# Optimization experiments

Hardware: AMD Instinct MI355X
Metric: run time of the kernel (lower is better)

The kernel has to match this reference:

```python
import jax, jax.numpy as jnp
import numpy as np

B, H, S, D = 2, 16, 2048, 64

def setup_inputs() -> dict:
    key = jax.random.key(0)
    kq, kk, kv = jax.random.split(key, 3)
    q = jax.random.normal(kq, (B, H, S, D), dtype=jnp.float32)
    k = jax.random.normal(kk, (B, H, S, D), dtype=jnp.float32)
    v = jax.random.normal(kv, (B, H, S, D), dtype=jnp.float32)
    # additive causal mask: 0 on/below diagonal, -1e9 above
    causal = jnp.tril(jnp.ones((S, S), dtype=bool))
    mask = jnp.where(causal, 0.0, -1e9).astype(jnp.float32)[None, None]
    return {"q": q, "k": k, "v": v, "mask": mask}

def reference(q, k, v, mask):
    # scores: [B,H,Sq,Sk]
    scale = 1.0 / jnp.sqrt(jnp.asarray(k.shape[-1], dtype=q.dtype))
    scores = jnp.einsum("bhqd,bhkd->bhqk", q, k) * scale
    scores = scores + mask
    attn = jax.nn.softmax(scores, axis=-1)
    return jnp.einsum("bhqk,bhkd->bhqd", attn, v)
```

## Files before the change

kernel.cpp:

```cpp
#include <hip/hip_runtime.h>
#include <hip/hip_bf16.h>


#define S_LEN 2048
#define D_DIM 64
#define BQ 64
#define BKV 64
#define NQT (S_LEN / BQ)
#define NBH 32

typedef __bf16 bf16x8 __attribute__((ext_vector_type(8)));
typedef __bf16 bf16x4 __attribute__((ext_vector_type(4)));
typedef float f32x4 __attribute__((ext_vector_type(4)));

#define QSCALE 0.1803368801111243f
#define NEG_INF (-1e30f)
#define THRLOG2 11.5f

__device__ inline void glds16(const void* g, void* l) {
    __builtin_amdgcn_global_load_lds(
        (const __attribute__((address_space(1))) unsigned int*)g,
        (__attribute__((address_space(3))) unsigned int*)l, 16, 0, 0);
}

__device__ inline float m3(float a, float b, float c) {
    return fmaxf(fmaxf(a, b), c);
}

__global__ __launch_bounds__(256)
void conv_fused_kernel(const float* __restrict__ k, const float* __restrict__ v,
                       __bf16* __restrict__ kb, __bf16* __restrict__ vt)
{
    __shared__ __bf16 T[64][72];
    const int bh = blockIdx.y, st = blockIdx.x;
    const int tid = threadIdx.x;
    const size_t base = (size_t)bh * S_LEN * D_DIM + (size_t)st * 64 * D_DIM;
    const float* kh = k + base;
    const float* vh = v + base;
    __bf16* kbh = kb + base;

#pragma unroll
    for (int it = 0; it < 2; ++it) {
        size_t i = ((size_t)tid + it * 256) * 8;
        float4 a = *(const float4*)(kh + i);
        float4 b = *(const float4*)(kh + i + 4);
        bf16x8 o;
        o[0] = (__bf16)a.x; o[1] = (__bf16)a.y; o[2] = (__bf16)a.z; o[3] = (__bf16)a.w;
        o[4] = (__bf16)b.x; o[5] = (__bf16)b.y; o[6] = (__bf16)b.z; o[7] = (__bf16)b.w;
        *(bf16x8*)(kbh + i) = o;
    }

#pragma unroll
    for (int it = 0; it < 4; ++it) {
        int idx = tid + it * 256;
        int s = idx >> 4, c4 = idx & 15;
        float4 f = *(const float4*)(vh + s * D_DIM + c4 * 4);
        T[c4 * 4 + 0][s] = (__bf16)f.x;
        T[c4 * 4 + 1][s] = (__bf16)f.y;
        T[c4 * 4 + 2][s] = (__bf16)f.z;
        T[c4 * 4 + 3][s] = (__bf16)f.w;
    }
    __syncthreads();
    __bf16* vth = vt + (size_t)bh * D_DIM * S_LEN + st * 64;
#pragma unroll
    for (int it = 0; it < 2; ++it) {
        int idx = tid + it * 256;
        int d = idx >> 3, c8 = idx & 7;
        int kk = c8 >> 2, g = c8 & 3;
        bf16x4 v0 = *(const bf16x4*)&T[d][kk * 32 + 4 * g];
        bf16x4 v1 = *(const bf16x4*)&T[d][kk * 32 + 16 + 4 * g];
        bf16x8 o;
        o[0] = v0[0]; o[1] = v0[1]; o[2] = v0[2]; o[3] = v0[3];
        o[4] = v1[0]; o[5] = v1[1]; o[6] = v1[2]; o[7] = v1[3];
        *(bf16x8*)(vth + (size_t)d * S_LEN + c8 * 8) = o;
    }
}


__global__ __launch_bounds__(256)
void attn_fwd_glds(const float* __restrict__ q, const __bf16* __restrict__ kb,
                   const __bf16* __restrict__ vt, float* __restrict__ out)
{
    __shared__ __bf16 KL[3][64][64];
    __shared__ __bf16 VL[3][64][64];

    const int tid  = threadIdx.x;
    const int w    = tid >> 6;
    const int lane = tid & 63;
    const int l15  = lane & 15;
    const int lg   = lane >> 4;

    const int p  = blockIdx.x;
    const int bh = blockIdx.y;

    const float*  qh = q  + (size_t)bh * S_LEN * D_DIM;
    const __bf16* kh = kb + (size_t)bh * S_LEN * D_DIM;
    const __bf16* vh = vt + (size_t)bh * D_DIM * S_LEN;
    float*        oh = out + (size_t)bh * S_LEN * D_DIM;

    int row_u[2], scol_u[2];
#pragma unroll
    for (int u = 0; u < 2; ++u) {
        int e = (u * 4 + w) * 512 + lane * 8;
        int r = e >> 6, c0 = e & 63;
        row_u[u]  = r;
        scol_u[u] = c0 ^ ((r & 7) << 3);
    }

#define STAGE(kt, buf)                                                          \
    {                                                                           \
        _Pragma("unroll")                                                       \
        for (int u = 0; u < 2; ++u) {                                           \
            glds16(kh + (size_t)((kt) * BKV + row_u[u]) * D_DIM + scol_u[u],    \
                   (__bf16*)&KL[buf][0][0] + (u * 4 + w) * 512);                \
            glds16(vh + (size_t)row_u[u] * S_LEN + (kt) * BKV + scol_u[u],      \
                   (__bf16*)&VL[buf][0][0] + (u * 4 + w) * 512);                \
        }                                                                       \
    }

    for (int half = 0; half < 2; ++half) {
        const int qtile = (half == 0) ? (NQT - 1 - p) : p;
        const int qbase = qtile * BQ;
        const int nt    = qtile + 1;

        bf16x8 qf[2];
        {
            const int qrow = qbase + w * 16 + l15;
            const float* qp = qh + (size_t)qrow * D_DIM + 8 * lg;
#pragma unroll
            for (int kk = 0; kk < 2; ++kk) {
                float4 a = *(const float4*)(qp + kk * 32);
                float4 b = *(const float4*)(qp + kk * 32 + 4);
                bf16x8 f;
                f[0] = (__bf16)(a.x * QSCALE); f[1] = (__bf16)(a.y * QSCALE);
                f[2] = (__bf16)(a.z * QSCALE); f[3] = (__bf16)(a.w * QSCALE);
                f[4] = (__bf16)(b.x * QSCALE); f[5] = (__bf16)(b.y * QSCALE);
                f[6] = (__bf16)(b.z * QSCALE); f[7] = (__bf16)(b.w * QSCALE);
                qf[kk] = f;
            }
        }

        f32x4 acc[4] = {};
        float m_run = NEG_INF;
        float l_part = 0.0f;

        if (half == 1) __syncthreads();
        STAGE(0, 0);
        if (nt > 1) STAGE(1, 1);

        for (int kt = 0; kt < nt; ++kt) {
            const int cur = kt % 3;
            if (kt + 1 < nt) { asm volatile("s_waitcnt vmcnt(4)" ::: "memory"); }
            else             { asm volatile("s_waitcnt vmcnt(0)" ::: "memory"); }
            __builtin_amdgcn_s_barrier();
            if (kt + 2 < nt) STAGE(kt + 2, (kt + 2) % 3);

            f32x4 s[4];
            __builtin_amdgcn_s_setprio(1);
#pragma unroll
            for (int jt = 0; jt < 4; ++jt) {
                const int j  = jt * 16 + l15;
                const int sw = (j & 7) << 3;
                f32x4 c = {};
#pragma unroll
                for (int kk = 0; kk < 2; ++kk) {
                    bf16x8 kf = *(const bf16x8*)&KL[cur][j][(kk * 32 + 8 * lg) ^ sw];
                    c = __builtin_amdgcn_mfma_f32_16x16x32_bf16(kf, qf[kk], c, 0, 0, 0);
                }
                s[jt] = c;
            }
            __builtin_amdgcn_s_setprio(0);

            if (kt == qtile) {
                const int qin = w * 16 + l15;
#pragma unroll
                for (int jt = 0; jt < 4; ++jt)
#pragma unroll
                    for (int r = 0; r < 4; ++r)
                        if (jt * 16 + 4 * lg + r > qin) s[jt][r] = NEG_INF;
            }

            float t0 = m3(s[0][0], s[0][1], s[0][2]);
            float t1 = m3(s[0][3], s[1][0], s[1][1]);
            float t2 = m3(s[1][2], s[1][3], s[2][0]);
            float t3 = m3(s[2][1], s[2][2], s[2][3]);
            float t4 = m3(s[3][0], s[3][1], s[3][2]);
            float mxl = m3(m3(t0, t1, t2), m3(t3, t4, s[3][3]), NEG_INF);

            if (__any(mxl > m_run + THRLOG2)) {
                float mx = fmaxf(mxl, __shfl_xor(mxl, 16));
                mx = fmaxf(mx, __shfl_xor(mx, 32));
                const float mt   = fmaxf(m_run, mx);
                const float corr = __builtin_amdgcn_exp2f(m_run - mt);
                l_part *= corr;
                m_run   = mt;
                float corr_a[4];
#pragma unroll
                for (int r = 0; r < 4; ++r) corr_a[r] = __shfl(corr, 4 * lg + r);
#pragma unroll
                for (int dt = 0; dt < 4; ++dt)
#pragma unroll
                    for (int r = 0; r < 4; ++r) acc[dt][r] *= corr_a[r];
            }

            float ps = 0.0f;
            float pe[4][4];
#pragma unroll
            for (int jt = 0; jt < 4; ++jt)
#pragma unroll
                for (int r = 0; r < 4; ++r) {
                    float e = __builtin_amdgcn_exp2f(s[jt][r] - m_run);
                    pe[jt][r] = e;
                    ps += e;
                }
            l_part += ps;

            bf16x8 pa[2];
#pragma unroll
            for (int kk = 0; kk < 2; ++kk)
#pragma unroll
                for (int i = 0; i < 4; ++i) {
                    pa[kk][i]     = (__bf16)pe[2 * kk][i];
                    pa[kk][4 + i] = (__bf16)pe[2 * kk + 1][i];
                }

            __builtin_amdgcn_s_setprio(1);
#pragma unroll
            for (int dt = 0; dt < 4; ++dt) {
                const int d  = dt * 16 + l15;
                const int sw = (d & 7) << 3;
#pragma unroll
                for (int kk = 0; kk < 2; ++kk) {
                    bf16x8 vb = *(const bf16x8*)&VL[cur][d][(kk * 32 + 8 * lg) ^ sw];
                    acc[dt] = __builtin_amdgcn_mfma_f32_16x16x32_bf16(pa[kk], vb, acc[dt], 0, 0, 0);
                }
            }
            __builtin_amdgcn_s_setprio(0);
        }

        float l_tot = l_part + __shfl_xor(l_part, 16);
        l_tot += __shfl_xor(l_tot, 32);
        float li_a[4];
#pragma unroll
        for (int r = 0; r < 4; ++r)
            li_a[r] = __builtin_amdgcn_rcpf(__shfl(l_tot, 4 * lg + r));
#pragma unroll
        for (int dt = 0; dt < 4; ++dt)
#pragma unroll
            for (int r = 0; r < 4; ++r)
                oh[(size_t)(qbase + w * 16 + 4 * lg + r) * D_DIM + dt * 16 + l15] =
                    acc[dt][r] * li_a[r];
    }
#undef STAGE
}


#define PAD 72
__global__ __launch_bounds__(256)
void attn_fwd_fallback(const float* __restrict__ q, const float* __restrict__ k,
                       const float* __restrict__ v, float* __restrict__ out)
{
    __shared__ __bf16 Klds[BKV][PAD];
    __shared__ __bf16 Vt[D_DIM][PAD];
    __shared__ __bf16 Plds[4][16][PAD];

    const int tid  = threadIdx.x;
    const int w    = tid >> 6;
    const int lane = tid & 63;
    const int l15  = lane & 15;
    const int lg   = lane >> 4;

    const int qtile = blockIdx.x;
    const int bh    = blockIdx.y;
    const int qbase = qtile * BQ;

    const size_t head_off = (size_t)bh * S_LEN * D_DIM;
    const float* qh = q + head_off;
    const float* kh = k + head_off;
    const float* vh = v + head_off;
    float*       oh = out + head_off;

    bf16x8 qf[2];
    {
        const int qrow = qbase + w * 16 + l15;
        const float* qp = qh + (size_t)qrow * D_DIM + 8 * lg;
#pragma unroll
        for (int c = 0; c < 2; ++c) {
            float4 a = *(const float4*)(qp + c * 32);
            float4 b = *(const float4*)(qp + c * 32 + 4);
            bf16x8 f;
            f[0] = (__bf16)(a.x * 0.125f); f[1] = (__bf16)(a.y * 0.125f);
            f[2] = (__bf16)(a.z * 0.125f); f[3] = (__bf16)(a.w * 0.125f);
            f[4] = (__bf16)(b.x * 0.125f); f[5] = (__bf16)(b.y * 0.125f);
            f[6] = (__bf16)(b.z * 0.125f); f[7] = (__bf16)(b.w * 0.125f);
            qf[c] = f;
        }
    }

    f32x4 acc[4] = {};
    float m_run[4], l_run[4];
#pragma unroll
    for (int r = 0; r < 4; ++r) { m_run[r] = -1e30f; l_run[r] = 0.0f; }

    const int nkv = qtile + 1;
    for (int kt = 0; kt < nkv; ++kt) {
        const int kv0 = kt * BKV;
        __syncthreads();
#pragma unroll
        for (int it = 0; it < 4; ++it) {
            int idx = tid + it * 256;
            int row = idx >> 4;
            int c4  = idx & 15;
            float4 kf = *(const float4*)(kh + (size_t)(kv0 + row) * D_DIM + c4 * 4);
            __bf16* kd = &Klds[row][c4 * 4];
            kd[0] = (__bf16)kf.x; kd[1] = (__bf16)kf.y;
            kd[2] = (__bf16)kf.z; kd[3] = (__bf16)kf.w;
            float4 vf = *(const float4*)(vh + (size_t)(kv0 + row) * D_DIM + c4 * 4);
            Vt[c4 * 4 + 0][row] = (__bf16)vf.x;
            Vt[c4 * 4 + 1][row] = (__bf16)vf.y;
            Vt[c4 * 4 + 2][row] = (__bf16)vf.z;
            Vt[c4 * 4 + 3][row] = (__bf16)vf.w;
        }
        __syncthreads();

        f32x4 sfrag[4];
#pragma unroll
        for (int kc = 0; kc < 4; ++kc) {
            bf16x8 kf0 = *(const bf16x8*)&Klds[kc * 16 + l15][8 * lg];
            bf16x8 kf1 = *(const bf16x8*)&Klds[kc * 16 + l15][32 + 8 * lg];
            f32x4 c = {};
            c = __builtin_amdgcn_mfma_f32_16x16x32_bf16(qf[0], kf0, c, 0, 0, 0);
            c = __builtin_amdgcn_mfma_f32_16x16x32_bf16(qf[1], kf1, c, 0, 0, 0);
            sfrag[kc] = c;
        }

        if (kt == qtile) {
#pragma unroll
            for (int kc = 0; kc < 4; ++kc) {
                const int j = kv0 + kc * 16 + l15;
#pragma unroll
                for (int r = 0; r < 4; ++r) {
                    const int qrow = qbase + w * 16 + lg * 4 + r;
                    if (j > qrow) sfrag[kc][r] = -1e30f;
                }
            }
        }

        float mt[4], corr[4], ps[4];
#pragma unroll
        for (int r = 0; r < 4; ++r) {
            float mx = fmaxf(fmaxf(sfrag[0][r], sfrag[1][r]),
                             fmaxf(sfrag[2][r], sfrag[3][r]));
            mx = fmaxf(mx, __shfl_xor(mx, 1));
            mx = fmaxf(mx, __shfl_xor(mx, 2));
            mx = fmaxf(mx, __shfl_xor(mx, 4));
            mx = fmaxf(mx, __shfl_xor(mx, 8));
            mt[r]   = fmaxf(m_run[r], mx);
            corr[r] = __expf(m_run[r] - mt[r]);
            ps[r]   = 0.0f;
        }
#pragma unroll
        for (int kc = 0; kc < 4; ++kc) {
#pragma unroll
            for (int r = 0; r < 4; ++r) {
                float pp = __expf(sfrag[kc][r] - mt[r]);
                ps[r] += pp;
                Plds[w][lg * 4 + r][kc * 16 + l15] = (__bf16)pp;
            }
        }
#pragma unroll
        for (int r = 0; r < 4; ++r) {
            ps[r] += __shfl_xor(ps[r], 1);
            ps[r] += __shfl_xor(ps[r], 2);
            ps[r] += __shfl_xor(ps[r], 4);
            ps[r] += __shfl_xor(ps[r], 8);
            l_run[r] = l_run[r] * corr[r] + ps[r];
            m_run[r] = mt[r];
        }
#pragma unroll
        for (int dt = 0; dt < 4; ++dt)
#pragma unroll
            for (int r = 0; r < 4; ++r)
                acc[dt][r] *= corr[r];

#pragma unroll
        for (int kk = 0; kk < 2; ++kk) {
            bf16x8 pf = *(const bf16x8*)&Plds[w][l15][kk * 32 + 8 * lg];
#pragma unroll
            for (int dt = 0; dt < 4; ++dt) {
                bf16x8 vf = *(const bf16x8*)&Vt[dt * 16 + l15][kk * 32 + 8 * lg];
                acc[dt] = __builtin_amdgcn_mfma_f32_16x16x32_bf16(pf, vf, acc[dt], 0, 0, 0);
            }
        }
    }

#pragma unroll
    for (int dt = 0; dt < 4; ++dt) {
#pragma unroll
        for (int r = 0; r < 4; ++r) {
            const int qrow = qbase + w * 16 + lg * 4 + r;
            oh[(size_t)qrow * D_DIM + dt * 16 + l15] = acc[dt][r] / l_run[r];
        }
    }
}

extern "C" void kernel_launch(void* const* d_in, const int* in_sizes, int n_in,
                              void* d_out, int out_size, void* d_ws, size_t ws_size,
                              hipStream_t stream) {
    const float* q = (const float*)d_in[0];
    const float* k = (const float*)d_in[1];
    const float* v = (const float*)d_in[2];
    float* out = (float*)d_out;

    const size_t kv_elems  = (size_t)NBH * S_LEN * D_DIM;
    const size_t ws_needed = kv_elems * 2 * sizeof(__bf16);

    if (ws_size >= ws_needed) {
        __bf16* kb = (__bf16*)d_ws;
        __bf16* vt = kb + kv_elems;
        conv_fused_kernel<<<dim3(S_LEN / 64, NBH), dim3(256), 0, stream>>>(k, v, kb, vt);
        attn_fwd_glds<<<dim3(NQT / 2, NBH), dim3(256), 0, stream>>>(q, kb, vt, out);
    } else {
        attn_fwd_fallback<<<dim3(NQT, NBH), dim3(256), 0, stream>>>(q, k, v, out);
    }
}
```

Baseline: 57.12 us.

## Split KV loop across two blocks per query tile and add combine kernel

Adds a split-KV path in which each query-tile pair is handled by two blocks, each taking alternating KV tiles (even or odd). Each block writes unnormalized partial outputs plus row max and sum to workspace. A new combine kernel then merges the two partials using log-sum-exp rescaling. This doubles the grid to 1024 blocks so more CUs are busy, at the cost of an extra launch, extra global traffic for the partials, and a shallower double-buffered prefetch with a full vmcnt(0) wait each iteration.

```diff
diff --git a/kernel.cpp b/kernel.cpp
--- a/kernel.cpp
+++ b/kernel.cpp
@@ -77,36 +77,6 @@
 }
 
 
-__global__ __launch_bounds__(256)
-void attn_fwd_glds(const float* __restrict__ q, const __bf16* __restrict__ kb,
-                   const __bf16* __restrict__ vt, float* __restrict__ out)
-{
-    __shared__ __bf16 KL[3][64][64];
-    __shared__ __bf16 VL[3][64][64];
-
-    const int tid  = threadIdx.x;
-    const int w    = tid >> 6;
-    const int lane = tid & 63;
-    const int l15  = lane & 15;
-    const int lg   = lane >> 4;
-
-    const int p  = blockIdx.x;
-    const int bh = blockIdx.y;
-
-    const float*  qh = q  + (size_t)bh * S_LEN * D_DIM;
-    const __bf16* kh = kb + (size_t)bh * S_LEN * D_DIM;
-    const __bf16* vh = vt + (size_t)bh * D_DIM * S_LEN;
-    float*        oh = out + (size_t)bh * S_LEN * D_DIM;
-
-    int row_u[2], scol_u[2];
-#pragma unroll
-    for (int u = 0; u < 2; ++u) {
-        int e = (u * 4 + w) * 512 + lane * 8;
-        int r = e >> 6, c0 = e & 63;
-        row_u[u]  = r;
-        scol_u[u] = c0 ^ ((r & 7) << 3);
-    }
-
 #define STAGE(kt, buf)                                                          \
     {                                                                           \
         _Pragma("unroll")                                                       \
@@ -118,10 +88,42 @@
         }                                                                       \
     }
 
+__global__ __launch_bounds__(256)
+void attn_fwd_split(const float* __restrict__ q, const __bf16* __restrict__ kb,
+                    const __bf16* __restrict__ vt, float* __restrict__ opart,
+                    float* __restrict__ ml)
+{
+    __shared__ __bf16 KL[2][64][64];
+    __shared__ __bf16 VL[2][64][64];
+
+    const int tid  = threadIdx.x;
+    const int w    = tid >> 6;
+    const int lane = tid & 63;
+    const int l15  = lane & 15;
+    const int lg   = lane >> 4;
+
+    const int ph = blockIdx.x;
+    const int p  = ph >> 1;
+    const int h  = ph & 1;
+    const int bh = blockIdx.y;
+
+    const float*  qh = q  + (size_t)bh * S_LEN * D_DIM;
+    const __bf16* kh = kb + (size_t)bh * S_LEN * D_DIM;
+    const __bf16* vh = vt + (size_t)bh * D_DIM * S_LEN;
+
+    int row_u[2], scol_u[2];
+#pragma unroll
+    for (int u = 0; u < 2; ++u) {
+        int e = (u * 4 + w) * 512 + lane * 8;
+        int r = e >> 6, c0 = e & 63;
+        row_u[u]  = r;
+        scol_u[u] = c0 ^ ((r & 7) << 3);
+    }
+
     for (int half = 0; half < 2; ++half) {
         const int qtile = (half == 0) ? (NQT - 1 - p) : p;
         const int qbase = qtile * BQ;
-        const int nt    = qtile + 1;
+        const int cnt   = (qtile >= h) ? (((qtile - h) >> 1) + 1) : 0;
 
         bf16x8 qf[2];
         {
@@ -145,15 +147,14 @@
         float l_part = 0.0f;
 
         if (half == 1) __syncthreads();
-        STAGE(0, 0);
-        if (nt > 1) STAGE(1, 1);
-
-        for (int kt = 0; kt < nt; ++kt) {
-            const int cur = kt % 3;
-            if (kt + 1 < nt) { asm volatile("s_waitcnt vmcnt(4)" ::: "memory"); }
-            else             { asm volatile("s_waitcnt vmcnt(0)" ::: "memory"); }
+        if (cnt > 0) STAGE(h, 0);
+
+        for (int i = 0; i < cnt; ++i) {
+            const int kt  = h + 2 * i;
+            const int cur = i & 1;
+            asm volatile("s_waitcnt vmcnt(0)" ::: "memory");
             __builtin_amdgcn_s_barrier();
-            if (kt + 2 < nt) STAGE(kt + 2, (kt + 2) % 3);
+            if (i + 1 < cnt) STAGE(kt + 2, cur ^ 1);
 
             f32x4 s[4];
             __builtin_amdgcn_s_setprio(1);
@@ -219,6 +220,211 @@
 #pragma unroll
             for (int kk = 0; kk < 2; ++kk)
 #pragma unroll
+                for (int i2 = 0; i2 < 4; ++i2) {
+                    pa[kk][i2]     = (__bf16)pe[2 * kk][i2];
+                    pa[kk][4 + i2] = (__bf16)pe[2 * kk + 1][i2];
+                }
+
+            __builtin_amdgcn_s_setprio(1);
+#pragma unroll
+            for (int dt = 0; dt < 4; ++dt) {
+                const int d  = dt * 16 + l15;
+                const int sw = (d & 7) << 3;
+#pragma unroll
+                for (int kk = 0; kk < 2; ++kk) {
+                    bf16x8 vb = *(const bf16x8*)&VL[cur][d][(kk * 32 + 8 * lg) ^ sw];
+                    acc[dt] = __builtin_amdgcn_mfma_f32_16x16x32_bf16(pa[kk], vb, acc[dt], 0, 0, 0);
+                }
+            }
+            __builtin_amdgcn_s_setprio(0);
+        }
+
+        float l_tot = l_part + __shfl_xor(l_part, 16);
+        l_tot += __shfl_xor(l_tot, 32);
+
+        float* op = opart + ((((size_t)bh * NQT + qtile) * 2 + h) << 12);
+#pragma unroll
+        for (int dt = 0; dt < 4; ++dt)
+#pragma unroll
+            for (int r = 0; r < 4; ++r)
+                op[(w * 16 + 4 * lg + r) * 64 + dt * 16 + l15] = acc[dt][r];
+
+        if (lg == 0) {
+            float* mlp = ml + ((((size_t)bh * NQT + qtile) * 2 + h) << 7);
+            mlp[w * 16 + l15]      = m_run;
+            mlp[64 + w * 16 + l15] = l_tot;
+        }
+    }
+}
+
+
+__global__ __launch_bounds__(256)
+void combine_kernel(const float* __restrict__ opart, const float* __restrict__ ml,
+                    float* __restrict__ out)
+{
+    const int qt  = blockIdx.x;
+    const int bh  = blockIdx.y;
+    const int tid = threadIdx.x;
+    const int row = tid >> 2;
+    const int c16 = (tid & 3) * 16;
+
+    const float* ml0 = ml + ((((size_t)bh * NQT + qt) * 2) << 7);
+    const float* ml1 = ml0 + 128;
+    const float m0 = ml0[row], l0 = ml0[64 + row];
+    const float m1 = ml1[row], l1 = ml1[64 + row];
+    const float M  = fmaxf(m0, m1);
+    const float w0 = __builtin_amdgcn_exp2f(m0 - M);
+    const float w1 = __builtin_amdgcn_exp2f(m1 - M);
+    const float li = __builtin_amdgcn_rcpf(w0 * l0 + w1 * l1);
+
+    const float* o0 = opart + ((((size_t)bh * NQT + qt) * 2) << 12) + row * 64 + c16;
+    const float* o1 = o0 + 4096;
+    float* oh = out + ((size_t)bh * S_LEN + qt * 64 + row) * D_DIM + c16;
+#pragma unroll
+    for (int c = 0; c < 4; ++c) {
+        float4 a = ((const float4*)o0)[c];
+        float4 b = ((const float4*)o1)[c];
+        float4 o;
+        o.x = (a.x * w0 + b.x * w1) * li;
+        o.y = (a.y * w0 + b.y * w1) * li;
+        o.z = (a.z * w0 + b.z * w1) * li;
+        o.w = (a.w * w0 + b.w * w1) * li;
+        ((float4*)oh)[c] = o;
+    }
+}
+
+
+__global__ __launch_bounds__(256)
+void attn_fwd_glds(const float* __restrict__ q, const __bf16* __restrict__ kb,
+                   const __bf16* __restrict__ vt, float* __restrict__ out)
+{
+    __shared__ __bf16 KL[3][64][64];
+    __shared__ __bf16 VL[3][64][64];
+
+    const int tid  = threadIdx.x;
+    const int w    = tid >> 6;
+    const int lane = tid & 63;
+    const int l15  = lane & 15;
+    const int lg   = lane >> 4;
+
+    const int p  = blockIdx.x;
+    const int bh = blockIdx.y;
+
+    const float*  qh = q  + (size_t)bh * S_LEN * D_DIM;
+    const __bf16* kh = kb + (size_t)bh * S_LEN * D_DIM;
+    const __bf16* vh = vt + (size_t)bh * D_DIM * S_LEN;
+    float*        oh = out + (size_t)bh * S_LEN * D_DIM;
+
+    int row_u[2], scol_u[2];
+#pragma unroll
+    for (int u = 0; u < 2; ++u) {
+        int e = (u * 4 + w) * 512 + lane * 8;
+        int r = e >> 6, c0 = e & 63;
+        row_u[u]  = r;
+        scol_u[u] = c0 ^ ((r & 7) << 3);
+    }
+
+    for (int half = 0; half < 2; ++half) {
+        const int qtile = (half == 0) ? (NQT - 1 - p) : p;
+        const int qbase = qtile * BQ;
+        const int nt    = qtile + 1;
+
+        bf16x8 qf[2];
+        {
+            const int qrow = qbase + w * 16 + l15;
+            const float* qp = qh + (size_t)qrow * D_DIM + 8 * lg;
+#pragma unroll
+            for (int kk = 0; kk < 2; ++kk) {
+                float4 a = *(const float4*)(qp + kk * 32);
+                float4 b = *(const float4*)(qp + kk * 32 + 4);
+                bf16x8 f;
+                f[0] = (__bf16)(a.x * QSCALE); f[1] = (__bf16)(a.y * QSCALE);
+                f[2] = (__bf16)(a.z * QSCALE); f[3] = (__bf16)(a.w * QSCALE);
+                f[4] = (__bf16)(b.x * QSCALE); f[5] = (__bf16)(b.y * QSCALE);
+                f[6] = (__bf16)(b.z * QSCALE); f[7] = (__bf16)(b.w * QSCALE);
+                qf[kk] = f;
+            }
+        }
+
+        f32x4 acc[4] = {};
+        float m_run = NEG_INF;
+        float l_part = 0.0f;
+
+        if (half == 1) __syncthreads();
+        STAGE(0, 0);
+        if (nt > 1) STAGE(1, 1);
+
+        for (int kt = 0; kt < nt; ++kt) {
+            const int cur = kt % 3;
+            if (kt + 1 < nt) { asm volatile("s_waitcnt vmcnt(4)" ::: "memory"); }
+            else             { asm volatile("s_waitcnt vmcnt(0)" ::: "memory"); }
+            __builtin_amdgcn_s_barrier();
+            if (kt + 2 < nt) STAGE(kt + 2, (kt + 2) % 3);
+
+            f32x4 s[4];
+            __builtin_amdgcn_s_setprio(1);
+#pragma unroll
+            for (int jt = 0; jt < 4; ++jt) {
+                const int j  = jt * 16 + l15;
+                const int sw = (j & 7) << 3;
+                f32x4 c = {};
+#pragma unroll
+                for (int kk = 0; kk < 2; ++kk) {
+                    bf16x8 kf = *(const bf16x8*)&KL[cur][j][(kk * 32 + 8 * lg) ^ sw];
+                    c = __builtin_amdgcn_mfma_f32_16x16x32_bf16(kf, qf[kk], c, 0, 0, 0);
+                }
+                s[jt] = c;
+            }
+            __builtin_amdgcn_s_setprio(0);
+
+            if (kt == qtile) {
+                const int qin = w * 16 + l15;
+#pragma unroll
+                for (int jt = 0; jt < 4; ++jt)
+#pragma unroll
+                    for (int r = 0; r < 4; ++r)
+                        if (jt * 16 + 4 * lg + r > qin) s[jt][r] = NEG_INF;
+            }
+
+            float t0 = m3(s[0][0], s[0][1], s[0][2]);
+            float t1 = m3(s[0][3], s[1][0], s[1][1]);
+            float t2 = m3(s[1][2], s[1][3], s[2][0]);
+            float t3 = m3(s[2][1], s[2][2], s[2][3]);
+            float t4 = m3(s[3][0], s[3][1], s[3][2]);
+            float mxl = m3(m3(t0, t1, t2), m3(t3, t4, s[3][3]), NEG_INF);
+
+            if (__any(mxl > m_run + THRLOG2)) {
+                float mx = fmaxf(mxl, __shfl_xor(mxl, 16));
+                mx = fmaxf(mx, __shfl_xor(mx, 32));
+                const float mt   = fmaxf(m_run, mx);
+                const float corr = __builtin_amdgcn_exp2f(m_run - mt);
+                l_part *= corr;
+                m_run   = mt;
+                float corr_a[4];
+#pragma unroll
+                for (int r = 0; r < 4; ++r) corr_a[r] = __shfl(corr, 4 * lg + r);
+#pragma unroll
+                for (int dt = 0; dt < 4; ++dt)
+#pragma unroll
+                    for (int r = 0; r < 4; ++r) acc[dt][r] *= corr_a[r];
+            }
+
+            float ps = 0.0f;
+            float pe[4][4];
+#pragma unroll
+            for (int jt = 0; jt < 4; ++jt)
+#pragma unroll
+                for (int r = 0; r < 4; ++r) {
+                    float e = __builtin_amdgcn_exp2f(s[jt][r] - m_run);
+                    pe[jt][r] = e;
+                    ps += e;
+                }
+            l_part += ps;
+
+            bf16x8 pa[2];
+#pragma unroll
+            for (int kk = 0; kk < 2; ++kk)
+#pragma unroll
                 for (int i = 0; i < 4; ++i) {
                     pa[kk][i]     = (__bf16)pe[2 * kk][i];
                     pa[kk][4 + i] = (__bf16)pe[2 * kk + 1][i];
@@ -251,8 +457,8 @@
                 oh[(size_t)(qbase + w * 16 + 4 * lg + r) * D_DIM + dt * 16 + l15] =
                     acc[dt][r] * li_a[r];
     }
+}
 #undef STAGE
-}
 
 
 #define PAD 72
@@ -260,7 +466,7 @@
 void attn_fwd_fallback(const float* __restrict__ q, const float* __restrict__ k,
                        const float* __restrict__ v, float* __restrict__ out)
 {
-    __shared__ __bf16 Klds[BKV][PAD];
+    __shared__ __bf16 Klds[64][PAD];
     __shared__ __bf16 Vt[D_DIM][PAD];
     __shared__ __bf16 Plds[4][16][PAD];
 
@@ -272,7 +478,7 @@
 
     const int qtile = blockIdx.x;
     const int bh    = blockIdx.y;
-    const int qbase = qtile * BQ;
+    const int qbase = qtile * 64;
 
     const size_t head_off = (size_t)bh * S_LEN * D_DIM;
     const float* qh = q + head_off;
@@ -304,7 +510,7 @@
 
     const int nkv = qtile + 1;
     for (int kt = 0; kt < nkv; ++kt) {
-        const int kv0 = kt * BKV;
+        const int kv0 = kt * 64;
         __syncthreads();
 #pragma unroll
         for (int it = 0; it < 4; ++it) {
@@ -412,15 +618,25 @@
     const float* v = (const float*)d_in[2];
     float* out = (float*)d_out;
 
-    const size_t kv_elems  = (size_t)NBH * S_LEN * D_DIM;
-    const size_t ws_needed = kv_elems * 2 * sizeof(__bf16);
-
-    if (ws_size >= ws_needed) {
+    const size_t kv_elems   = (size_t)NBH * S_LEN * D_DIM;
+    const size_t conv_bytes = kv_elems * 2 * sizeof(__bf16);
+    const size_t op_bytes   = (size_t)NBH * NQT * 2 * 4096 * 4;
+    const size_t ml_bytes   = (size_t)NBH * NQT * 2 * 128 * 4;
+
+    if (ws_size >= conv_bytes + op_bytes + ml_bytes) {
+        __bf16* kb = (__bf16*)d_ws;
+        __bf16* vt = kb + kv_elems;
+        float* opart = (float*)((char*)d_ws + conv_bytes);
+        float* ml    = (float*)((char*)d_ws + conv_bytes + op_bytes);
+        conv_fused_kernel<<<dim3(S_LEN / 64, NBH), dim3(256), 0, stream>>>(k, v, kb, vt);
+        attn_fwd_split<<<dim3(32, NBH), dim3(256), 0, stream>>>(q, kb, vt, opart, ml);
+        combine_kernel<<<dim3(NQT, NBH), dim3(256), 0, stream>>>(opart, ml, out);
+    } else if (ws_size >= conv_bytes) {
         __bf16* kb = (__bf16*)d_ws;
         __bf16* vt = kb + kv_elems;
         conv_fused_kernel<<<dim3(S_LEN / 64, NBH), dim3(256), 0, stream>>>(k, v, kb, vt);
         attn_fwd_glds<<<dim3(NQT / 2, NBH), dim3(256), 0, stream>>>(q, kb, vt, out);
     } else {
-        attn_fwd_fallback<<<dim3(NQT, NBH), dim3(256), 0, stream>>>(q, k, v, out);
-    }
-}
+        attn_fwd_fallback<<<dim3(S_LEN / 64, NBH), dim3(256), 0, stream>>>(q, k, v, out);
+    }
+}
```

New measurement: 60.33 us. 5.6% more time.
